# Kernel optimization log

Hardware: AMD Instinct MI355X
Metric: run time of the kernel (lower is better)

The kernel has to match this reference:

```python
import jax, jax.numpy as jnp
import numpy as np

B, S, D, H = 4, 2048, 512, 8
DK = D // H


def setup_inputs() -> dict:
    key = jax.random.key(0)
    ks = jax.random.split(key, 12)
    s = 0.02
    return {
        "q": jax.random.normal(ks[0], (B, S, D), jnp.float32),
        "k": jax.random.normal(ks[1], (B, S, D), jnp.float32),
        "v": jax.random.normal(ks[2], (B, S, D), jnp.float32),
        "mask": jax.random.randint(ks[3], (B, 1, S, S), 0, 2, jnp.int32),
        "Wq": jax.random.normal(ks[4], (D, D), jnp.float32) * s,
        "bq": jnp.zeros((D,), jnp.float32),
        "Wk": jax.random.normal(ks[5], (D, D), jnp.float32) * s,
        "bk": jnp.zeros((D,), jnp.float32),
        "Wv": jax.random.normal(ks[6], (D, D), jnp.float32) * s,
        "bv": jnp.zeros((D,), jnp.float32),
        "Wo": jax.random.normal(ks[7], (D, D), jnp.float32) * s,
        "bo": jnp.zeros((D,), jnp.float32),
    }


def reference(q, k, v, mask, Wq, bq, Wk, bk, Wv, bv, Wo, bo):
    # Linear projections (torch Linear: x @ W.T + b)
    qh = (q @ Wq.T + bq).reshape(B, S, H, DK).transpose(0, 2, 1, 3)  # [B,H,S,dk]
    kh = (k @ Wk.T + bk).reshape(B, S, H, DK).transpose(0, 2, 1, 3)
    vh = (v @ Wv.T + bv).reshape(B, S, H, DK).transpose(0, 2, 1, 3)
    # FAITHFUL quirk: original divides by q.shape[1] AFTER transpose == num_heads
    scores = jnp.einsum("bhqd,bhkd->bhqk", qh, kh) / H  # [B,H,S,S]
    scores = jnp.where(mask == 0, jnp.float32(-1e9), scores)
    attn = jax.nn.softmax(scores, axis=-1)
    ctx = jnp.einsum("bhqk,bhkd->bhqd", attn, vh)  # [B,H,S,dk]
    x = ctx.transpose(0, 2, 1, 3).reshape(B, S, D)
    return x @ Wo.T + bo  # dropout is identity in eval mode
```

## Files before the change

kernel.cpp:

```cpp
#include <hip/hip_runtime.h>
#include <math.h>

constexpr int Bc  = 4;
constexpr int Sc  = 2048;
constexpr int Dc  = 512;
constexpr int Hc  = 8;
constexpr int DKc = 64;
constexpr int Mc  = Bc * Sc;

constexpr float SCALE_Q = 0.180336880111120426f;

typedef __attribute__((ext_vector_type(8)))  short s16x8;
typedef __attribute__((ext_vector_type(4)))  float f32x4;
typedef __attribute__((ext_vector_type(16))) float f32x16;

__device__ __forceinline__ unsigned short f2bf(float f) {
    __bf16 h = (__bf16)f;
    return __builtin_bit_cast(unsigned short, h);
}

__device__ __forceinline__ float fexp2(float x) {
#if __has_builtin(__builtin_amdgcn_exp2f)
    return __builtin_amdgcn_exp2f(x);
#else
    return __expf(x * 0.6931471805599453f);
#endif
}

__device__ __forceinline__ uint4 pack8(float4 a, float4 b) {
    uint4 u;
    u.x = (unsigned)f2bf(a.x) | ((unsigned)f2bf(a.y) << 16);
    u.y = (unsigned)f2bf(a.z) | ((unsigned)f2bf(a.w) << 16);
    u.z = (unsigned)f2bf(b.x) | ((unsigned)f2bf(b.y) << 16);
    u.w = (unsigned)f2bf(b.z) | ((unsigned)f2bf(b.w) << 16);
    return u;
}

__global__ __launch_bounds__(256)
void pack_mask(const int* __restrict__ mask, unsigned long long* __restrict__ out,
               int nwords)
{
    int gw   = (blockIdx.x * blockDim.x + threadIdx.x) >> 6;
    int lane = threadIdx.x & 63;
    int nw   = (gridDim.x * blockDim.x) >> 6;
    for (int w0 = gw * 4; w0 < nwords; w0 += nw * 4) {
        int vals[4];
#pragma unroll
        for (int c = 0; c < 4; ++c)
            vals[c] = mask[(size_t)(w0 + c) * 64 + lane];
#pragma unroll
        for (int c = 0; c < 4; ++c) {
            unsigned long long bits = __ballot(vals[c] != 0);
            if (lane == 0) out[w0 + c] = bits;
        }
    }
}

__global__ __launch_bounds__(256)
void cvt4(const float* __restrict__ i0, const float* __restrict__ i1,
          const float* __restrict__ i2, const float* __restrict__ i3,
          unsigned short* __restrict__ o0, unsigned short* __restrict__ o1,
          unsigned short* __restrict__ o2, unsigned short* __restrict__ o3,
          int n4)
{
    const float* in; unsigned short* out;
    switch (blockIdx.y) {
        case 0: in = i0; out = o0; break;
        case 1: in = i1; out = o1; break;
        case 2: in = i2; out = o2; break;
        default: in = i3; out = o3; break;
    }
    int i = blockIdx.x * 256 + threadIdx.x;
    if (i < n4) {
        float4 v = ((const float4*)in)[i];
        ushort4 r;
        r.x = f2bf(v.x); r.y = f2bf(v.y); r.z = f2bf(v.z); r.w = f2bf(v.w);
        ((ushort4*)out)[i] = r;
    }
}

template<bool XBF>
__global__ __launch_bounds__(256, 3)
void gemm128(const void* __restrict__ x0, const void* __restrict__ x1,
             const void* __restrict__ x2,
             const unsigned short* __restrict__ w0, const unsigned short* __restrict__ w1,
             const unsigned short* __restrict__ w2,
             const float* __restrict__ b0, const float* __restrict__ b1,
             const float* __restrict__ b2,
             void* __restrict__ o0v, void* __restrict__ o1v, void* __restrict__ o2v,
             float s0, float s1, float s2, int m0, int m1, int m2)
{
    const void* Xv; const unsigned short* W; const float* bias; void* outv;
    float scale; int mode;
    switch (blockIdx.z) {
        case 0:  Xv = x0; W = w0; bias = b0; outv = o0v; scale = s0; mode = m0; break;
        case 1:  Xv = x1; W = w1; bias = b1; outv = o1v; scale = s1; mode = m1; break;
        default: Xv = x2; W = w2; bias = b2; outv = o2v; scale = s2; mode = m2; break;
    }

    __shared__ unsigned short Xs[2][128 * 64];
    __shared__ unsigned short Ws[2][64 * 64];

    const int tid = threadIdx.x;
    const int w = tid >> 6, lane = tid & 63, ln = lane & 15, qd = lane >> 4;
    const int wm = (w >> 1) * 64, wn = (w & 1) * 32;
    const int row0 = blockIdx.x * 128, col0 = blockIdx.y * 64;

    f32x4 acc[4][2];
#pragma unroll
    for (int mt = 0; mt < 4; ++mt)
#pragma unroll
        for (int nt = 0; nt < 2; ++nt) acc[mt][nt] = f32x4{0.f, 0.f, 0.f, 0.f};

    uint4 xb[4], wr[2];
    auto load = [&](int k0) {
#pragma unroll
        for (int c = 0; c < 4; ++c) {
            int u = tid + c * 256, r = u >> 3, c8 = u & 7;
            if (XBF) {
                xb[c] = *(const uint4*)((const unsigned short*)Xv +
                                        (size_t)(row0 + r) * 512 + k0 + c8 * 8);
            } else {
                const float* xp = (const float*)Xv + (size_t)(row0 + r) * 512 + k0 + c8 * 8;
                xb[c] = pack8(*(const float4*)xp, *(const float4*)(xp + 4));
            }
        }
#pragma unroll
        for (int c = 0; c < 2; ++c) {
            int u = tid + c * 256, r = u >> 3, c8 = u & 7;
            wr[c] = *(const uint4*)(W + (size_t)(col0 + r) * 512 + k0 + c8 * 8);
        }
    };
    auto store = [&](int buf) {
#pragma unroll
        for (int c = 0; c < 4; ++c) {
            int u = tid + c * 256, r = u >> 3, c8 = u & 7;
            *(uint4*)&Xs[buf][r * 64 + ((c8 ^ (r & 7)) * 8)] = xb[c];
        }
#pragma unroll
        for (int c = 0; c < 2; ++c) {
            int u = tid + c * 256, r = u >> 3, c8 = u & 7;
            *(uint4*)&Ws[buf][r * 64 + ((c8 ^ (r & 7)) * 8)] = wr[c];
        }
    };

    load(0);
    store(0);
    for (int k0 = 0; k0 < 512; k0 += 64) {
        const int buf = (k0 >> 6) & 1;
        __syncthreads();
        if (k0 + 64 < 512) load(k0 + 64);
#pragma unroll
        for (int kc = 0; kc < 2; ++kc) {
            s16x8 af[4], bfr[2];
#pragma unroll
            for (int mt = 0; mt < 4; ++mt) {
                int r = wm + mt * 16 + ln;
                af[mt] = *(const s16x8*)&Xs[buf][r * 64 + (((kc * 4 + qd) ^ (ln & 7)) * 8)];
            }
#pragma unroll
            for (int nt = 0; nt < 2; ++nt) {
                int r = wn + nt * 16 + ln;
                bfr[nt] = *(const s16x8*)&Ws[buf][r * 64 + (((kc * 4 + qd) ^ (ln & 7)) * 8)];
            }
#pragma unroll
            for (int mt = 0; mt < 4; ++mt)
#pragma unroll
                for (int nt = 0; nt < 2; ++nt)
                    acc[mt][nt] = __builtin_amdgcn_mfma_f32_16x16x32_bf16(
                        af[mt], bfr[nt], acc[mt][nt], 0, 0, 0);
        }
        if (k0 + 64 < 512) store(buf ^ 1);
    }

#pragma unroll
    for (int nt = 0; nt < 2; ++nt) {
        const int n = col0 + wn + nt * 16 + ln;
        const float bz = bias[n];
#pragma unroll
        for (int mt = 0; mt < 4; ++mt) {
            const int mbase = row0 + wm + mt * 16 + qd * 4;
            if (mode == 0) {
                float* o = (float*)outv;
#pragma unroll
                for (int r = 0; r < 4; ++r)
                    o[(size_t)(mbase + r) * 512 + n] = acc[mt][nt][r] + bz;
            } else if (mode == 1) {
                unsigned short* o = (unsigned short*)outv;
                const int h = n >> 6, dk = n & 63;
#pragma unroll
                for (int r = 0; r < 4; ++r) {
                    int m = mbase + r, b = m >> 11, s = m & 2047;
                    o[((size_t)(b * Hc + h) * Sc + s) * 64 + dk] =
                        f2bf((acc[mt][nt][r] + bz) * scale);
                }
            } else {
                unsigned short* o = (unsigned short*)outv;
                const int h = n >> 6, dk = n & 63;
                const int b = mbase >> 11, sb = mbase & 2047;
                const int ss = (sb & ~12) | ((sb & 4) << 1) | ((sb & 8) >> 1);
                ushort4 pk;
                pk.x = f2bf((acc[mt][nt][0] + bz) * scale);
                pk.y = f2bf((acc[mt][nt][1] + bz) * scale);
                pk.z = f2bf((acc[mt][nt][2] + bz) * scale);
                pk.w = f2bf((acc[mt][nt][3] + bz) * scale);
                *(ushort4*)(o + ((size_t)(b * Hc + h) * 64 + dk) * Sc + ss) = pk;
            }
        }
    }
}

__global__ __launch_bounds__(256, 3)
void attn_mfma(const unsigned short* __restrict__ qh, const unsigned short* __restrict__ kh,
               const unsigned short* __restrict__ vt, const unsigned* __restrict__ mbits,
               unsigned short* __restrict__ ctx)
{
    __shared__ uint4 smem4[2][1024];

    const int bh = blockIdx.y, b = bh >> 3, h = bh & 7;
    const int q0 = blockIdx.x * 64;
    const int tid = threadIdx.x;
    const int w = tid >> 6;
    const int g = w >> 1;
    const int kh_ = w & 1;
    const int lane = tid & 63, ln = lane & 31, hf = lane >> 5;
    const int wv = tid >> 7;
    const int qr = q0 + g * 32 + ln;

    s16x8 qf[4];
    {
        const unsigned short* qp = qh + ((size_t)bh * Sc + qr) * 64 + hf * 8;
#pragma unroll
        for (int kc = 0; kc < 4; ++kc)
            qf[kc] = *(const s16x8*)(qp + kc * 16);
    }

    f32x16 o0, o1;
#pragma unroll
    for (int r = 0; r < 16; ++r) { o0[r] = 0.f; o1[r] = 0.f; }
    float lr = 0.f;

    const unsigned* mr = mbits + ((size_t)b * Sc + qr) * (Sc / 32);
    const unsigned short* kbase = kh + (size_t)bh * Sc * 64;
    const unsigned short* vbase = vt + (size_t)bh * 64 * Sc;

    const int kt0 = kh_ * 1024;

    auto stage_tile = [&](int buf, int kt) {
        char* gb = (char*)smem4[buf] + kh_ * 8192;
#pragma unroll
        for (int c = 0; c < 2; ++c) {
            const int seg = wv * 2 + c;
            const int s   = seg * 64 + lane;
            const int r   = s >> 3, cc = (s & 7) ^ (r & 7);
            const unsigned short* gs = kbase + (size_t)(kt + r) * 64 + cc * 8;
            __builtin_amdgcn_global_load_lds(
                (const __attribute__((address_space(1))) unsigned int*)gs,
                (__attribute__((address_space(3))) unsigned int*)(gb + seg * 1024),
                16, 0, 0);
        }
        char* vb = gb + 4096;
#pragma unroll
        for (int c = 0; c < 2; ++c) {
            const int seg = wv * 2 + c;
            const int dv  = lane ^ (seg << 1);
            const unsigned short* gs = vbase + (size_t)dv * Sc + kt + seg * 8;
            __builtin_amdgcn_global_load_lds(
                (const __attribute__((address_space(1))) unsigned int*)gs,
                (__attribute__((address_space(3))) unsigned int*)(vb + seg * 1024),
                16, 0, 0);
        }
    };

    stage_tile(0, kt0);
    unsigned mwn = mr[kt0 >> 5];

    for (int i = 0; i < 32; ++i) {
        const int kt = kt0 + i * 32;
        const int buf = i & 1;
        __syncthreads();
        const unsigned mw = mwn;
        if (i < 31) {
            stage_tile(buf ^ 1, kt + 32);
            mwn = mr[(kt + 32) >> 5];
        }

        const unsigned short* Ks = (const unsigned short*)smem4[buf] + kh_ * 4096;
        const unsigned short* Vs = Ks + 2048;

        f32x16 sv;
#pragma unroll
        for (int r = 0; r < 16; ++r) sv[r] = 0.f;
        __builtin_amdgcn_s_setprio(1);
#pragma unroll
        for (int kc = 0; kc < 4; ++kc) {
            s16x8 kf = *(const s16x8*)&Ks[ln * 64 + ((((kc << 1) | hf) ^ (ln & 7)) * 8)];
            sv = __builtin_amdgcn_mfma_f32_32x32x16_bf16(kf, qf[kc], sv, 0, 0, 0);
        }
        __builtin_amdgcn_s_setprio(0);

        float ps = 0.f;
        unsigned pu[8];
#pragma unroll
        for (int r = 0; r < 16; r += 2) {
            int key0 = (r & 3) + 8 * (r >> 2) + 4 * hf;
            int key1 = ((r + 1) & 3) + 8 * ((r + 1) >> 2) + 4 * hf;
            float a0 = ((mw >> key0) & 1u) ? sv[r]     : -1e9f;
            float a1 = ((mw >> key1) & 1u) ? sv[r + 1] : -1e9f;
            float p0 = fexp2(a0), p1 = fexp2(a1);
            ps += p0 + p1;
            pu[r >> 1] = (unsigned)f2bf(p0) | ((unsigned)f2bf(p1) << 16);
        }
        lr += ps;

        __builtin_amdgcn_s_setprio(1);
#pragma unroll
        for (int kc = 0; kc < 2; ++kc) {
            uint4 ua; ua.x = pu[4*kc]; ua.y = pu[4*kc+1]; ua.z = pu[4*kc+2]; ua.w = pu[4*kc+3];
            s16x8 pf = __builtin_bit_cast(s16x8, ua);
            const int cc = (kc << 1) | hf;
            s16x8 v0  = *(const s16x8*)&Vs[(cc * 64 + (ln ^ (cc << 1))) * 8];
            s16x8 v1  = *(const s16x8*)&Vs[(cc * 64 + ((32 + ln) ^ (cc << 1))) * 8];
            o0 = __builtin_amdgcn_mfma_f32_32x32x16_bf16(v0, pf, o0, 0, 0, 0);
            o1 = __builtin_amdgcn_mfma_f32_32x32x16_bf16(v1, pf, o1, 0, 0, 0);
        }
        __builtin_amdgcn_s_setprio(0);
    }

    lr += __shfl_xor(lr, 32);

    __syncthreads();
    float* cs = (float*)smem4[0];
    const int row = g * 64 + lane;
    float* my = cs + (size_t)row * 48;
    const int sw = lane & 7;
    if (kh_ == 1) {
#pragma unroll
        for (int r = 0; r < 4; ++r) {
            *(float4*)(my + ((r ^ sw) * 4))       = make_float4(o0[4*r], o0[4*r+1], o0[4*r+2], o0[4*r+3]);
            *(float4*)(my + (((r + 4) ^ sw) * 4)) = make_float4(o1[4*r], o1[4*r+1], o1[4*r+2], o1[4*r+3]);
        }
        my[32] = lr;
    }
    __syncthreads();
    if (kh_ == 0) {
        lr += my[32];
        const float inv = 1.f / lr;
#pragma unroll
        for (int r = 0; r < 4; ++r) {
            float4 a0 = *(const float4*)(my + ((r ^ sw) * 4));
            float4 a1 = *(const float4*)(my + (((r + 4) ^ sw) * 4));
            o0[4*r]   = (o0[4*r]   + a0.x) * inv; o0[4*r+1] = (o0[4*r+1] + a0.y) * inv;
            o0[4*r+2] = (o0[4*r+2] + a0.z) * inv; o0[4*r+3] = (o0[4*r+3] + a0.w) * inv;
            o1[4*r]   = (o1[4*r]   + a1.x) * inv; o1[4*r+1] = (o1[4*r+1] + a1.y) * inv;
            o1[4*r+2] = (o1[4*r+2] + a1.z) * inv; o1[4*r+3] = (o1[4*r+3] + a1.w) * inv;
        }
        unsigned short* op = ctx + ((size_t)(b * Sc + qr)) * 512 + h * 64;
#pragma unroll
        for (int gg = 0; gg < 4; ++gg) {
            ushort4 a, c;
            a.x = f2bf(o0[gg*4+0]); a.y = f2bf(o0[gg*4+1]);
            a.z = f2bf(o0[gg*4+2]); a.w = f2bf(o0[gg*4+3]);
            c.x = f2bf(o1[gg*4+0]); c.y = f2bf(o1[gg*4+1]);
            c.z = f2bf(o1[gg*4+2]); c.w = f2bf(o1[gg*4+3]);
            *(ushort4*)(op + 8 * gg + 4 * hf)      = a;
            *(ushort4*)(op + 32 + 8 * gg + 4 * hf) = c;
        }
    }
}

extern "C" void kernel_launch(void* const* d_in, const int* in_sizes, int n_in,
                              void* d_out, int out_size, void* d_ws, size_t ws_size,
                              hipStream_t stream)
{
    (void)in_sizes; (void)n_in; (void)out_size; (void)ws_size;

    const float* q    = (const float*)d_in[0];
    const float* k    = (const float*)d_in[1];
    const float* v    = (const float*)d_in[2];
    const int*   mask = (const int*)  d_in[3];
    const float* Wq   = (const float*)d_in[4];
    const float* bq   = (const float*)d_in[5];
    const float* Wk   = (const float*)d_in[6];
    const float* bk   = (const float*)d_in[7];
    const float* Wv   = (const float*)d_in[8];
    const float* bv   = (const float*)d_in[9];
    const float* Wo   = (const float*)d_in[10];
    const float* bo   = (const float*)d_in[11];
    float* out = (float*)d_out;

    constexpr size_t TEN = (size_t)Bc * Hc * Sc * DKc;
    char* p = (char*)d_ws;
    unsigned short* wqb   = (unsigned short*)p;  p += (size_t)Dc * Dc * 2;
    unsigned short* wkb   = (unsigned short*)p;  p += (size_t)Dc * Dc * 2;
    unsigned short* wvb   = (unsigned short*)p;  p += (size_t)Dc * Dc * 2;
    unsigned short* wob   = (unsigned short*)p;  p += (size_t)Dc * Dc * 2;
    unsigned short* qh_bf = (unsigned short*)p;  p += TEN * 2;
    unsigned short* kh_bf = (unsigned short*)p;  p += TEN * 2;
    unsigned short* vt_bf = (unsigned short*)p;  p += TEN * 2;
    unsigned short* ctx   = (unsigned short*)p;  p += TEN * 2;
    unsigned long long* mb64 = (unsigned long long*)p;

    const int nwords = Bc * Sc * (Sc / 64);

    dim3 bb(256);

    pack_mask<<<dim3(16384), bb, 0, stream>>>(mask, mb64, nwords);
    cvt4<<<dim3(Dc * Dc / 4 / 256, 4), bb, 0, stream>>>(Wq, Wk, Wv, Wo, wqb, wkb, wvb, wob,
                                                        Dc * Dc / 4);
    gemm128<false><<<dim3(Mc / 128, Dc / 64, 3), bb, 0, stream>>>(
        q, k, v, wqb, wkb, wvb, bq, bk, bv, qh_bf, kh_bf, vt_bf,
        SCALE_Q, 1.0f, 1.0f, 1, 1, 2);
    attn_mfma<<<dim3(Sc / 64, Bc * Hc), bb, 0, stream>>>(qh_bf, kh_bf, vt_bf,
                                                         (const unsigned*)mb64, ctx);
    gemm128<true><<<dim3(Mc / 128, Dc / 64, 1), bb, 0, stream>>>(
        ctx, ctx, ctx, wob, wob, wob, bo, bo, bo, out, out, out,
        1.0f, 1.0f, 1.0f, 0, 0, 0);
}
```

Before: 323.6 us.

## Pre-convert activations to bf16 and stage GEMM tiles via direct global-to-LDS loads

```diff
diff --git a/kernel.cpp b/kernel.cpp
--- a/kernel.cpp
+++ b/kernel.cpp
@@ -25,15 +25,6 @@
 #else
     return __expf(x * 0.6931471805599453f);
 #endif
-}
-
-__device__ __forceinline__ uint4 pack8(float4 a, float4 b) {
-    uint4 u;
-    u.x = (unsigned)f2bf(a.x) | ((unsigned)f2bf(a.y) << 16);
-    u.y = (unsigned)f2bf(a.z) | ((unsigned)f2bf(a.w) << 16);
-    u.z = (unsigned)f2bf(b.x) | ((unsigned)f2bf(b.y) << 16);
-    u.w = (unsigned)f2bf(b.z) | ((unsigned)f2bf(b.w) << 16);
-    return u;
 }
 
 __global__ __launch_bounds__(256)
@@ -79,10 +70,9 @@
     }
 }
 
-template<bool XBF>
 __global__ __launch_bounds__(256, 3)
-void gemm128(const void* __restrict__ x0, const void* __restrict__ x1,
-             const void* __restrict__ x2,
+void gemm128(const unsigned short* __restrict__ x0, const unsigned short* __restrict__ x1,
+             const unsigned short* __restrict__ x2,
              const unsigned short* __restrict__ w0, const unsigned short* __restrict__ w1,
              const unsigned short* __restrict__ w2,
              const float* __restrict__ b0, const float* __restrict__ b1,
@@ -90,12 +80,12 @@
              void* __restrict__ o0v, void* __restrict__ o1v, void* __restrict__ o2v,
              float s0, float s1, float s2, int m0, int m1, int m2)
 {
-    const void* Xv; const unsigned short* W; const float* bias; void* outv;
+    const unsigned short* X; const unsigned short* W; const float* bias; void* outv;
     float scale; int mode;
     switch (blockIdx.z) {
-        case 0:  Xv = x0; W = w0; bias = b0; outv = o0v; scale = s0; mode = m0; break;
-        case 1:  Xv = x1; W = w1; bias = b1; outv = o1v; scale = s1; mode = m1; break;
-        default: Xv = x2; W = w2; bias = b2; outv = o2v; scale = s2; mode = m2; break;
+        case 0:  X = x0; W = w0; bias = b0; outv = o0v; scale = s0; mode = m0; break;
+        case 1:  X = x1; W = w1; bias = b1; outv = o1v; scale = s1; mode = m1; break;
+        default: X = x2; W = w2; bias = b2; outv = o2v; scale = s2; mode = m2; break;
     }
 
     __shared__ unsigned short Xs[2][128 * 64];
@@ -112,44 +102,36 @@
 #pragma unroll
         for (int nt = 0; nt < 2; ++nt) acc[mt][nt] = f32x4{0.f, 0.f, 0.f, 0.f};
 
-    uint4 xb[4], wr[2];
-    auto load = [&](int k0) {
+    auto stage = [&](int buf, int k0) {
 #pragma unroll
         for (int c = 0; c < 4; ++c) {
-            int u = tid + c * 256, r = u >> 3, c8 = u & 7;
-            if (XBF) {
-                xb[c] = *(const uint4*)((const unsigned short*)Xv +
-                                        (size_t)(row0 + r) * 512 + k0 + c8 * 8);
-            } else {
-                const float* xp = (const float*)Xv + (size_t)(row0 + r) * 512 + k0 + c8 * 8;
-                xb[c] = pack8(*(const float4*)xp, *(const float4*)(xp + 4));
-            }
+            const int s = c * 256 + w * 64 + lane;
+            const int r = s >> 3, cc = (s & 7) ^ (r & 7);
+            const unsigned short* gs = X + (size_t)(row0 + r) * 512 + k0 + cc * 8;
+            __builtin_amdgcn_global_load_lds(
+                (const __attribute__((address_space(1))) unsigned int*)gs,
+                (__attribute__((address_space(3))) unsigned int*)
+                    ((char*)&Xs[buf][0] + (c * 256 + w * 64) * 16),
+                16, 0, 0);
         }
 #pragma unroll
         for (int c = 0; c < 2; ++c) {
-            int u = tid + c * 256, r = u >> 3, c8 = u & 7;
-            wr[c] = *(const uint4*)(W + (size_t)(col0 + r) * 512 + k0 + c8 * 8);
+            const int s = c * 256 + w * 64 + lane;
+            const int r = s >> 3, cc = (s & 7) ^ (r & 7);
+            const unsigned short* gs = W + (size_t)(col0 + r) * 512 + k0 + cc * 8;
+            __builtin_amdgcn_global_load_lds(
+                (const __attribute__((address_space(1))) unsigned int*)gs,
+                (__attribute__((address_space(3))) unsigned int*)
+                    ((char*)&Ws[buf][0] + (c * 256 + w * 64) * 16),
+                16, 0, 0);
         }
     };
-    auto store = [&](int buf) {
-#pragma unroll
-        for (int c = 0; c < 4; ++c) {
-            int u = tid + c * 256, r = u >> 3, c8 = u & 7;
-            *(uint4*)&Xs[buf][r * 64 + ((c8 ^ (r & 7)) * 8)] = xb[c];
-        }
-#pragma unroll
-        for (int c = 0; c < 2; ++c) {
-            int u = tid + c * 256, r = u >> 3, c8 = u & 7;
-            *(uint4*)&Ws[buf][r * 64 + ((c8 ^ (r & 7)) * 8)] = wr[c];
-        }
-    };
-
-    load(0);
-    store(0);
+
+    stage(0, 0);
     for (int k0 = 0; k0 < 512; k0 += 64) {
         const int buf = (k0 >> 6) & 1;
         __syncthreads();
-        if (k0 + 64 < 512) load(k0 + 64);
+        if (k0 + 64 < 512) stage(buf ^ 1, k0 + 64);
 #pragma unroll
         for (int kc = 0; kc < 2; ++kc) {
             s16x8 af[4], bfr[2];
@@ -170,7 +152,6 @@
                     acc[mt][nt] = __builtin_amdgcn_mfma_f32_16x16x32_bf16(
                         af[mt], bfr[nt], acc[mt][nt], 0, 0, 0);
         }
-        if (k0 + 64 < 512) store(buf ^ 1);
     }
 
 #pragma unroll
@@ -401,6 +382,10 @@
     unsigned short* ctx   = (unsigned short*)p;  p += TEN * 2;
     unsigned long long* mb64 = (unsigned long long*)p;
 
+    unsigned short* qb = (unsigned short*)d_out;
+    unsigned short* kb = qb + TEN;
+    unsigned short* vb = ctx;
+
     const int nwords = Bc * Sc * (Sc / 64);
 
     dim3 bb(256);
@@ -408,12 +393,14 @@
     pack_mask<<<dim3(16384), bb, 0, stream>>>(mask, mb64, nwords);
     cvt4<<<dim3(Dc * Dc / 4 / 256, 4), bb, 0, stream>>>(Wq, Wk, Wv, Wo, wqb, wkb, wvb, wob,
                                                         Dc * Dc / 4);
-    gemm128<false><<<dim3(Mc / 128, Dc / 64, 3), bb, 0, stream>>>(
-        q, k, v, wqb, wkb, wvb, bq, bk, bv, qh_bf, kh_bf, vt_bf,
+    cvt4<<<dim3((int)(TEN / 4 / 256), 3), bb, 0, stream>>>(q, k, v, v, qb, kb, vb, vb,
+                                                           (int)(TEN / 4));
+    gemm128<<<dim3(Mc / 128, Dc / 64, 3), bb, 0, stream>>>(
+        qb, kb, vb, wqb, wkb, wvb, bq, bk, bv, qh_bf, kh_bf, vt_bf,
         SCALE_Q, 1.0f, 1.0f, 1, 1, 2);
     attn_mfma<<<dim3(Sc / 64, Bc * Hc), bb, 0, stream>>>(qh_bf, kh_bf, vt_bf,
                                                          (const unsigned*)mb64, ctx);
-    gemm128<true><<<dim3(Mc / 128, Dc / 64, 1), bb, 0, stream>>>(
+    gemm128<<<dim3(Mc / 128, Dc / 64, 1), bb, 0, stream>>>(
         ctx, ctx, ctx, wob, wob, wob, bo, bo, bo, out, out, out,
         1.0f, 1.0f, 1.0f, 0, 0, 0);
 }
```

New measurement: 268.1 us. 1.21x faster.
